# Performance work log

Hardware: AMD Instinct MI355X
Metric: run time of the kernel (lower is better)

## Reference

```python
import jax, jax.numpy as jnp
import numpy as np
from jax import lax

VOCAB = 5000
BLANK = 0          # vocab.unk_id
SMOOTHING = 0.1    # config.model.label_smoothing
ALPHA = 0.2        # config.model.alpha
NEG = -1e30        # finite stand-in for -inf (stable under logaddexp)


def setup_inputs() -> dict:
    key = jax.random.key(0)
    k1, k2, k3 = jax.random.split(key, 3)
    att_logits = jax.random.normal(k1, (16, 128, VOCAB), dtype=jnp.float32)
    ctc_logits = jax.random.normal(k2, (16, 512, VOCAB), dtype=jnp.float32)
    targets = jax.random.randint(k3, (16, 128), 0, VOCAB)
    return {"att_logits": att_logits, "ctc_logits": ctc_logits, "targets": targets}


def _label_smoothing_loss(logit_bsv, targets_bs):
    # torch: label_smoothed filled with smoothing/(V-1), confidence at target;
    # loss = mean over rows of sum(-label_smoothed * logit).
    B, S, V = logit_bsv.shape
    logit = logit_bsv.reshape(-1, V)                       # (B*S, V)
    tgt = targets_bs.reshape(-1)                           # (B*S,)
    confidence = 1.0 - SMOOTHING
    off = SMOOTHING / (V - 1)
    tgt_logit = jnp.take_along_axis(logit, tgt[:, None], axis=1)[:, 0]
    row_sum = jnp.sum(logit, axis=-1)
    # sum(-ls*logit) = -(confidence*logit[t] + off*(row_sum - logit[t]))
    per_row = -(confidence * tgt_logit + off * (row_sum - tgt_logit))
    return jnp.mean(per_row)


def _ctc_loss(log_probs_btv, targets_bs):
    # torch nn.CTCLoss(blank=BLANK, reduction='mean', zero_infinity=True)
    # input is time-major log-probs (T, B, V); full lengths on both sides.
    lp = jnp.transpose(log_probs_btv, (1, 0, 2))           # (T, B, V)
    T, B, V = lp.shape
    S = targets_bs.shape[1]
    L = 2 * S + 1
    # extended target: blank interleaved
    ext = jnp.full((B, L), BLANK, dtype=targets_bs.dtype).at[:, 1::2].set(targets_bs)
    # emission log-probs per extended symbol: (T, B, L)
    emit = jnp.take_along_axis(lp, jnp.broadcast_to(ext[None], (T, B, L)), axis=2)
    # skip (s-2) transition allowed when ext[s] != blank and ext[s] != ext[s-2]
    ext_m2 = jnp.roll(ext, 2, axis=1)
    allow2 = (ext != BLANK) & (ext != ext_m2)
    allow2 = allow2.at[:, :2].set(False)
    alpha0 = jnp.full((B, L), NEG, dtype=lp.dtype)
    alpha0 = alpha0.at[:, 0].set(emit[0, :, 0]).at[:, 1].set(emit[0, :, 1])

    negpad1 = jnp.full((B, 1), NEG, dtype=lp.dtype)
    negpad2 = jnp.full((B, 2), NEG, dtype=lp.dtype)

    def step(alpha, e_t):
        a1 = jnp.concatenate([negpad1, alpha[:, :-1]], axis=1)
        a2 = jnp.concatenate([negpad2, alpha[:, :-2]], axis=1)
        a2 = jnp.where(allow2, a2, NEG)
        new = jnp.logaddexp(jnp.logaddexp(alpha, a1), a2) + e_t
        return new, None

    alphaT, _ = lax.scan(step, alpha0, emit[1:])
    ll = jnp.logaddexp(alphaT[:, L - 1], alphaT[:, L - 2])
    loss_b = -ll                                           # (B,)
    # zero_infinity: invalid paths (loss ~ 1e30) -> 0
    loss_b = jnp.where(loss_b > 1e20, 0.0, loss_b)
    # reduction='mean': divide by target length, then mean over batch
    return jnp.mean(loss_b / S)


def reference(att_logits, ctc_logits, targets):
    att_loss = _label_smoothing_loss(att_logits, targets)
    ctc_loss = _ctc_loss(ctc_logits, targets)
    return ALPHA * att_loss + (1.0 - ALPHA) * ctc_loss
```

## Files before the change

kernel.cpp:

```cpp
#include <hip/hip_runtime.h>
#include <math.h>

#define VOCAB   5000
#define T_CTC   512
#define S_TGT   128
#define BATCH   16
#define ALPHA_W 0.2f
#define CONF    0.9f
#define OFFV    (0.1f / 4999.0f)
#define CHUNK   64
#define NCHUNK  8
#define CSTR    132
#define ATT_N   (BATCH * S_TGT)
#define WS_OFF  4096
#define GATHER_BLKS (BATCH * (T_CTC / 2))

__global__ __launch_bounds__(256)
void gather_att_kernel(const float* __restrict__ ctc,
                       const float* __restrict__ att,
                       const int*   __restrict__ tgt,
                       float*       __restrict__ ws)
{
    if (blockIdx.x < GATHER_BLKS) {
        const int b     = blockIdx.x >> 8;
        const int tpair = blockIdx.x & 255;
        const int t0    = 2 * tpair;

        __shared__ int tg[S_TGT];
        if (threadIdx.x < S_TGT) tg[threadIdx.x] = tgt[b * S_TGT + threadIdx.x];
        __syncthreads();

        const float* lp   = ctc + (size_t)b * T_CTC * VOCAB;
        float*       cbuf = ws + WS_OFF + ((size_t)b * T_CTC) * CSTR;

        for (int v = threadIdx.x; v < 258; v += 256) {
            const int tt  = (v < 129) ? 0 : 1;
            const int idx = (v < 129) ? v : v - 129;
            const int col = (idx < 128) ? tg[idx] : 0;
            cbuf[(size_t)(t0 + tt) * CSTR + idx] = lp[(size_t)(t0 + tt) * VOCAB + col];
        }
        return;
    }

    const int rr = blockIdx.x - GATHER_BLKS;
    const float* row = att + (size_t)rr * VOCAB;
    const float4* row4 = (const float4*)row;

    float sum = 0.0f;
    for (int i = threadIdx.x; i < VOCAB / 4; i += 256) {
        float4 v = row4[i];
        sum += v.x + v.y + v.z + v.w;
    }
    #pragma unroll
    for (int off = 32; off > 0; off >>= 1)
        sum += __shfl_down(sum, off, 64);

    __shared__ float wsum[4];
    if ((threadIdx.x & 63) == 0) wsum[threadIdx.x >> 6] = sum;
    __syncthreads();
    if (threadIdx.x == 0) {
        const float rs = wsum[0] + wsum[1] + wsum[2] + wsum[3];
        const float tl = row[tgt[rr]];
        ws[rr] = -(CONF * tl + OFFV * (rs - tl));
    }
}

__global__ __launch_bounds__(512)
void ctc_kernel(const int* __restrict__ tgt, float* __restrict__ ws)
{
    __shared__ __align__(16) float ebuf[2][CHUNK][CSTR];

    const int b    = blockIdx.x;
    const int tid  = threadIdx.x;
    const int wave = tid >> 6;
    const int lane = tid & 63;
    const int*   tg   = tgt + b * S_TGT;
    const float* cbuf = ws + WS_OFF + ((size_t)b * T_CTC) * CSTR;

    {
        const float4* src = (const float4*)(cbuf + (size_t)1 * CSTR);
        float4*       dst = (float4*)&ebuf[0][0][0];
        for (int i = tid; i < CHUNK * (CSTR / 4); i += 512) dst[i] = src[i];
    }

    const int k  = lane;
    const int t1 = tg[2 * k];
    const int t3 = tg[2 * k + 1];
    const int tp = (k > 0) ? tg[2 * k - 1] : 0;
    const double g1 = ((k > 0) && (t1 != 0) && (t1 != tp)) ? 1.0 : 0.0;
    const double g3 = ((t3 != 0) && (t3 != t1)) ? 1.0 : 0.0;

    const float e00 = cbuf[128];
    double M  = (double)e00;
    double b0 = (k == 0) ? 1.0 : 0.0;
    double b1 = (k == 0) ? (double)__expf(cbuf[0] - e00) : 0.0;
    double b2 = 0.0, b3 = 0.0, b4 = 0.0;

    __syncthreads();

    for (int c = 0; c < NCHUNK; ++c) {
        const int buf = c & 1;
        if (wave == 0) {
            const int tbase = 1 + c * CHUNK;
            #pragma unroll
            for (int h = 0; h < CHUNK / 16; ++h) {
                double X1[16], X3[16];
                float  Z[16];
                #pragma unroll
                for (int i = 0; i < 16; ++i) {
                    const int st = h * 16 + i;
                    const float2 e13 = *reinterpret_cast<const float2*>(&ebuf[buf][st][2 * k]);
                    const float  e0  = ebuf[buf][st][128];
                    X1[i] = (double)__expf(e13.x - e0);
                    X3[i] = (double)__expf(e13.y - e0);
                    Z[i]  = e0;
                }
                #pragma unroll
                for (int i = 0; i < 16; ++i) {
                    if (tbase + h * 16 + i < T_CTC) {
                        double p3 = __shfl_up(b3, 1, 64);
                        p3 = (k == 0) ? 0.0 : p3;
                        const double n0 = b0 + p3;
                        const double n1 = (b1 + b0 + g1 * p3) * X1[i];
                        const double n2 = b2 + b1;
                        const double n3 = (b3 + b2 + g3 * b1) * X3[i];
                        const double n4 = b4 + b3;
                        b0 = n0; b1 = n1; b2 = n2; b3 = n3; b4 = n4;
                        M += (double)Z[i];
                    }
                }
            }
        } else if (c + 1 < NCHUNK) {
            const int nbuf  = buf ^ 1;
            const int tbase = 1 + (c + 1) * CHUNK;
            const int rows  = min(CHUNK, T_CTC - tbase);
            const float4* src = (const float4*)(cbuf + (size_t)tbase * CSTR);
            float4*       dst = (float4*)&ebuf[nbuf][0][0];
            const int n4v = rows * (CSTR / 4);
            for (int i = tid - 64; i < n4v; i += 448) dst[i] = src[i];
        }
        __syncthreads();
    }

    if (wave == 0 && k == 63) {
        const double bsum = b3 + b4;
        const double ll   = M + log(bsum);
        float loss_b = (float)(-ll);
        if (!(loss_b <= 1e20f)) loss_b = 0.0f;
        ws[ATT_N + b] = loss_b;
    }
}

__global__ __launch_bounds__(256)
void combine_kernel(const float* __restrict__ ws, float* __restrict__ out)
{
    const int tid = threadIdx.x;
    float s_att = 0.0f;
    for (int i = tid; i < ATT_N; i += 256) s_att += ws[i];
    float s_ctc = (tid < BATCH) ? ws[ATT_N + tid] : 0.0f;

    #pragma unroll
    for (int off = 32; off > 0; off >>= 1) {
        s_att += __shfl_down(s_att, off, 64);
        s_ctc += __shfl_down(s_ctc, off, 64);
    }
    __shared__ float wa[4], wc[4];
    if ((tid & 63) == 0) { wa[tid >> 6] = s_att; wc[tid >> 6] = s_ctc; }
    __syncthreads();
    if (tid == 0) {
        const float inv = 1.0f / (float)ATT_N;
        const float a = (wa[0] + wa[1] + wa[2] + wa[3]) * inv;
        const float c = (wc[0] + wc[1] + wc[2] + wc[3]) * inv;
        out[0] = ALPHA_W * a + (1.0f - ALPHA_W) * c;
    }
}

extern "C" void kernel_launch(void* const* d_in, const int* in_sizes, int n_in,
                              void* d_out, int out_size, void* d_ws, size_t ws_size,
                              hipStream_t stream)
{
    const float* att = (const float*)d_in[0];
    const float* ctc = (const float*)d_in[1];
    const int*   tgt = (const int*)d_in[2];
    float* out = (float*)d_out;
    float* ws  = (float*)d_ws;

    gather_att_kernel<<<GATHER_BLKS + ATT_N, 256, 0, stream>>>(ctc, att, tgt, ws);
    ctc_kernel<<<BATCH, 512, 0, stream>>>(tgt, ws);
    combine_kernel<<<1, 256, 0, stream>>>(ws, out);
}
```

Measured before the change: 283.7 us.

## Overlap att row sums with CTC recursion and use DPP shift with register prefetch

The attention row-sum blocks move from the gather kernel into the CTC kernel, so they can run on idle CUs while the 16 serial CTC waves execute. The CTC recursion now uses a single wave per batch item. It replaces the LDS double buffer and block barriers with direct register prefetch from global memory, ping-ponging between two 16-step buffers. The lane shift uses a DPP row_shr-style update instead of a shuffle. The gather kernel is coarsened to 16 timesteps per block. The risks are exposed global-load latency in the serial chain and whether the DPP control (0x138, likely wave_shr) shifts correctly across all 64 lanes.

```diff
diff --git a/kernel.cpp b/kernel.cpp
--- a/kernel.cpp
+++ b/kernel.cpp
@@ -8,141 +8,146 @@
 #define ALPHA_W 0.2f
 #define CONF    0.9f
 #define OFFV    (0.1f / 4999.0f)
-#define CHUNK   64
-#define NCHUNK  8
 #define CSTR    132
 #define ATT_N   (BATCH * S_TGT)
 #define WS_OFF  4096
-#define GATHER_BLKS (BATCH * (T_CTC / 2))
+#define TCH     16
+#define GATHER_BLKS (BATCH * (T_CTC / TCH))
+
+__device__ __forceinline__ double dpp_shr1(double x)
+{
+    const int lo  = __double2loint(x);
+    const int hi  = __double2hiint(x);
+    const int slo = __builtin_amdgcn_update_dpp(0, lo, 0x138, 0xF, 0xF, true);
+    const int shi = __builtin_amdgcn_update_dpp(0, hi, 0x138, 0xF, 0xF, true);
+    return __hiloint2double(shi, slo);
+}
 
 __global__ __launch_bounds__(256)
-void gather_att_kernel(const float* __restrict__ ctc,
-                       const float* __restrict__ att,
-                       const int*   __restrict__ tgt,
-                       float*       __restrict__ ws)
+void gather_kernel(const float* __restrict__ ctc, const int* __restrict__ tgt,
+                   float* __restrict__ ws)
 {
-    if (blockIdx.x < GATHER_BLKS) {
-        const int b     = blockIdx.x >> 8;
-        const int tpair = blockIdx.x & 255;
-        const int t0    = 2 * tpair;
+    const int b = blockIdx.x >> 5;
+    const int c = blockIdx.x & 31;
 
-        __shared__ int tg[S_TGT];
-        if (threadIdx.x < S_TGT) tg[threadIdx.x] = tgt[b * S_TGT + threadIdx.x];
+    __shared__ int tg[S_TGT];
+    if (threadIdx.x < S_TGT) tg[threadIdx.x] = tgt[b * S_TGT + threadIdx.x];
+    __syncthreads();
+
+    const float* lp   = ctc + ((size_t)b * T_CTC + (size_t)c * TCH) * VOCAB;
+    float*       cbuf = ws + WS_OFF + ((size_t)b * T_CTC + (size_t)c * TCH) * CSTR;
+
+    #pragma unroll
+    for (int p = 0; p < TCH / 2; ++p) {
+        for (int v = threadIdx.x; v < 258; v += 256) {
+            const int tt  = (v < 129) ? (2 * p) : (2 * p + 1);
+            const int idx = (v < 129) ? v : v - 129;
+            const int col = (idx < S_TGT) ? tg[idx] : 0;
+            cbuf[(size_t)tt * CSTR + idx] = lp[(size_t)tt * VOCAB + col];
+        }
+    }
+}
+
+__device__ __forceinline__ void prefetch16(const float* __restrict__ cbuf,
+                                           int base, int k, float2* E, float* Z)
+{
+    #pragma unroll
+    for (int i = 0; i < 16; ++i) {
+        int t = base + i;
+        t = (t < T_CTC) ? t : (T_CTC - 1);
+        const float* row = cbuf + (size_t)t * CSTR;
+        E[i] = *reinterpret_cast<const float2*>(row + 2 * k);
+        Z[i] = row[S_TGT];
+    }
+}
+
+template<bool TAIL>
+__device__ __forceinline__ void run16(const float2* E, const float* Z, int base,
+                                      double& b0, double& b1, double& b2,
+                                      double& b3, double& b4, double& M,
+                                      const double g1, const double g3)
+{
+    #pragma unroll
+    for (int i = 0; i < 16; ++i) {
+        if (TAIL && (base + i >= T_CTC)) return;
+        const float  e0 = Z[i];
+        const double X1 = (double)__expf(E[i].x - e0);
+        const double X3 = (double)__expf(E[i].y - e0);
+        const double p3 = dpp_shr1(b3);
+        const double n0 = b0 + p3;
+        const double n1 = (b1 + b0 + g1 * p3) * X1;
+        const double n2 = b2 + b1;
+        const double n3 = (b3 + b2 + g3 * b1) * X3;
+        const double n4 = b4 + b3;
+        b0 = n0; b1 = n1; b2 = n2; b3 = n3; b4 = n4;
+        M += (double)e0;
+    }
+}
+
+__global__ __launch_bounds__(256)
+void ctc_att_kernel(const int* __restrict__ tgt, const float* __restrict__ att,
+                    float* __restrict__ ws)
+{
+    if (blockIdx.x >= BATCH) {
+        const int rr = blockIdx.x - BATCH;
+        const float* row = att + (size_t)rr * VOCAB;
+        const float4* row4 = (const float4*)row;
+
+        float sum = 0.0f;
+        for (int i = threadIdx.x; i < VOCAB / 4; i += 256) {
+            float4 v = row4[i];
+            sum += v.x + v.y + v.z + v.w;
+        }
+        #pragma unroll
+        for (int off = 32; off > 0; off >>= 1)
+            sum += __shfl_down(sum, off, 64);
+
+        __shared__ float wsum[4];
+        if ((threadIdx.x & 63) == 0) wsum[threadIdx.x >> 6] = sum;
         __syncthreads();
-
-        const float* lp   = ctc + (size_t)b * T_CTC * VOCAB;
-        float*       cbuf = ws + WS_OFF + ((size_t)b * T_CTC) * CSTR;
-
-        for (int v = threadIdx.x; v < 258; v += 256) {
-            const int tt  = (v < 129) ? 0 : 1;
-            const int idx = (v < 129) ? v : v - 129;
-            const int col = (idx < 128) ? tg[idx] : 0;
-            cbuf[(size_t)(t0 + tt) * CSTR + idx] = lp[(size_t)(t0 + tt) * VOCAB + col];
+        if (threadIdx.x == 0) {
+            const float rs = wsum[0] + wsum[1] + wsum[2] + wsum[3];
+            const float tl = row[tgt[rr]];
+            ws[rr] = -(CONF * tl + OFFV * (rs - tl));
         }
         return;
     }
 
-    const int rr = blockIdx.x - GATHER_BLKS;
-    const float* row = att + (size_t)rr * VOCAB;
-    const float4* row4 = (const float4*)row;
+    if (threadIdx.x >= 64) return;
+    const int b = blockIdx.x;
+    const int k = threadIdx.x;
+    const int*   tg   = tgt + b * S_TGT;
+    const float* cbuf = ws + WS_OFF + (size_t)b * T_CTC * CSTR;
 
-    float sum = 0.0f;
-    for (int i = threadIdx.x; i < VOCAB / 4; i += 256) {
-        float4 v = row4[i];
-        sum += v.x + v.y + v.z + v.w;
-    }
-    #pragma unroll
-    for (int off = 32; off > 0; off >>= 1)
-        sum += __shfl_down(sum, off, 64);
-
-    __shared__ float wsum[4];
-    if ((threadIdx.x & 63) == 0) wsum[threadIdx.x >> 6] = sum;
-    __syncthreads();
-    if (threadIdx.x == 0) {
-        const float rs = wsum[0] + wsum[1] + wsum[2] + wsum[3];
-        const float tl = row[tgt[rr]];
-        ws[rr] = -(CONF * tl + OFFV * (rs - tl));
-    }
-}
-
-__global__ __launch_bounds__(512)
-void ctc_kernel(const int* __restrict__ tgt, float* __restrict__ ws)
-{
-    __shared__ __align__(16) float ebuf[2][CHUNK][CSTR];
-
-    const int b    = blockIdx.x;
-    const int tid  = threadIdx.x;
-    const int wave = tid >> 6;
-    const int lane = tid & 63;
-    const int*   tg   = tgt + b * S_TGT;
-    const float* cbuf = ws + WS_OFF + ((size_t)b * T_CTC) * CSTR;
-
-    {
-        const float4* src = (const float4*)(cbuf + (size_t)1 * CSTR);
-        float4*       dst = (float4*)&ebuf[0][0][0];
-        for (int i = tid; i < CHUNK * (CSTR / 4); i += 512) dst[i] = src[i];
-    }
-
-    const int k  = lane;
     const int t1 = tg[2 * k];
     const int t3 = tg[2 * k + 1];
     const int tp = (k > 0) ? tg[2 * k - 1] : 0;
     const double g1 = ((k > 0) && (t1 != 0) && (t1 != tp)) ? 1.0 : 0.0;
     const double g3 = ((t3 != 0) && (t3 != t1)) ? 1.0 : 0.0;
 
-    const float e00 = cbuf[128];
+    const float e00 = cbuf[S_TGT];
     double M  = (double)e00;
     double b0 = (k == 0) ? 1.0 : 0.0;
     double b1 = (k == 0) ? (double)__expf(cbuf[0] - e00) : 0.0;
     double b2 = 0.0, b3 = 0.0, b4 = 0.0;
 
-    __syncthreads();
+    float2 EA[16], EB[16];
+    float  ZA[16], ZB[16];
 
-    for (int c = 0; c < NCHUNK; ++c) {
-        const int buf = c & 1;
-        if (wave == 0) {
-            const int tbase = 1 + c * CHUNK;
-            #pragma unroll
-            for (int h = 0; h < CHUNK / 16; ++h) {
-                double X1[16], X3[16];
-                float  Z[16];
-                #pragma unroll
-                for (int i = 0; i < 16; ++i) {
-                    const int st = h * 16 + i;
-                    const float2 e13 = *reinterpret_cast<const float2*>(&ebuf[buf][st][2 * k]);
-                    const float  e0  = ebuf[buf][st][128];
-                    X1[i] = (double)__expf(e13.x - e0);
-                    X3[i] = (double)__expf(e13.y - e0);
-                    Z[i]  = e0;
-                }
-                #pragma unroll
-                for (int i = 0; i < 16; ++i) {
-                    if (tbase + h * 16 + i < T_CTC) {
-                        double p3 = __shfl_up(b3, 1, 64);
-                        p3 = (k == 0) ? 0.0 : p3;
-                        const double n0 = b0 + p3;
-                        const double n1 = (b1 + b0 + g1 * p3) * X1[i];
-                        const double n2 = b2 + b1;
-                        const double n3 = (b3 + b2 + g3 * b1) * X3[i];
-                        const double n4 = b4 + b3;
-                        b0 = n0; b1 = n1; b2 = n2; b3 = n3; b4 = n4;
-                        M += (double)Z[i];
-                    }
-                }
-            }
-        } else if (c + 1 < NCHUNK) {
-            const int nbuf  = buf ^ 1;
-            const int tbase = 1 + (c + 1) * CHUNK;
-            const int rows  = min(CHUNK, T_CTC - tbase);
-            const float4* src = (const float4*)(cbuf + (size_t)tbase * CSTR);
-            float4*       dst = (float4*)&ebuf[nbuf][0][0];
-            const int n4v = rows * (CSTR / 4);
-            for (int i = tid - 64; i < n4v; i += 448) dst[i] = src[i];
+    prefetch16(cbuf, 1, k, EA, ZA);
+    for (int h2 = 0; h2 < 16; ++h2) {
+        const int base0 = 1 + 32 * h2;
+        prefetch16(cbuf, base0 + 16, k, EB, ZB);
+        run16<false>(EA, ZA, base0, b0, b1, b2, b3, b4, M, g1, g3);
+        if (h2 < 15) {
+            prefetch16(cbuf, base0 + 32, k, EA, ZA);
+            run16<false>(EB, ZB, base0 + 16, b0, b1, b2, b3, b4, M, g1, g3);
+        } else {
+            run16<true>(EB, ZB, base0 + 16, b0, b1, b2, b3, b4, M, g1, g3);
         }
-        __syncthreads();
     }
 
-    if (wave == 0 && k == 63) {
+    if (k == 63) {
         const double bsum = b3 + b4;
         const double ll   = M + log(bsum);
         float loss_b = (float)(-ll);
@@ -185,7 +190,7 @@
     float* out = (float*)d_out;
     float* ws  = (float*)d_ws;
 
-    gather_att_kernel<<<GATHER_BLKS + ATT_N, 256, 0, stream>>>(ctc, att, tgt, ws);
-    ctc_kernel<<<BATCH, 512, 0, stream>>>(tgt, ws);
+    gather_kernel<<<GATHER_BLKS, 256, 0, stream>>>(ctc, tgt, ws);
+    ctc_att_kernel<<<BATCH + ATT_N, 256, 0, stream>>>(tgt, att, ws);
     combine_kernel<<<1, 256, 0, stream>>>(ws, out);
 }
```

New measurement: 279.7 us. About the same (-1.4%).
